# Optimization experiments

Hardware: AMD Instinct MI355X
Metric: run time of the kernel (lower is better)

The kernel has to match this reference:

```python
import jax, jax.numpy as jnp
import numpy as np

N_ATOMS = 16384
N_BLOCKS = 4096
K = 3          # top-k nearest context atoms (min(3, n_ctx) in original; n_ctx >> 3 here)
EPS_W = 1e-8   # inverse-distance weight epsilon (matches original)
EPS_D = 1e-12  # tiny epsilon inside sqrt for numerical safety of the distance


def setup_inputs() -> dict:
    key = jax.random.key(0)
    k1, k2, k3, k4, k5 = jax.random.split(key, 5)
    # coordinates spread out like real molecular coords (Angstrom-ish scale)
    X = jax.random.normal(k1, (N_ATOMS, 3), dtype=jnp.float32) * 10.0
    base_noise = jax.random.normal(k2, (N_ATOMS, 3), dtype=jnp.float32)      # randn_like(X)
    centroid_noise = jax.random.normal(k3, (N_ATOMS, 3), dtype=jnp.float32)  # per-atom randn(3)
    block_ids = jnp.sort(jax.random.randint(k4, (N_ATOMS,), 0, N_BLOCKS)).astype(jnp.int32)
    generate_mask = jax.random.randint(k5, (N_BLOCKS,), 0, 2).astype(bool)
    return {
        "X": X,
        "base_noise": base_noise,
        "centroid_noise": centroid_noise,
        "block_ids": block_ids,
        "generate_mask": generate_mask,
    }


def reference(X, base_noise, centroid_noise, block_ids, generate_mask):
    """Vectorized sample_chemical_prior: for every generated atom, find the 3
    nearest CONTEXT atoms, take an inverse-distance-weighted centroid, and add
    0.5 * gaussian noise. Non-generated atoms keep base_noise (randn_like)."""
    n = X.shape[0]
    gen_atoms = generate_mask[block_ids]           # [N] atoms being generated
    ctx = ~gen_atoms                               # [N] context atoms

    # pairwise squared distances via ||a||^2 + ||b||^2 - 2 a.b  -> [N, N]
    xn = jnp.sum(X * X, axis=-1)
    sq = xn[:, None] + xn[None, :] - 2.0 * (X @ X.T)
    d = jnp.sqrt(jnp.maximum(sq, 0.0) + EPS_D)

    # only context atoms are valid neighbor candidates; exclude self for safety
    not_self = ~jnp.eye(n, dtype=bool)
    d = jnp.where(ctx[None, :] & not_self, d, jnp.inf)

    # k nearest context atoms per row (smallest distances)
    neg_dk, idx = jax.lax.top_k(-d, K)             # [N, K]
    dk = -neg_dk

    # inverse-distance weights, normalized (matches original)
    w = 1.0 / (dk + EPS_W)
    w = w / jnp.sum(w, axis=-1, keepdims=True)

    coords = X[idx]                                # [N, K, 3] gather neighbor coords
    centroid = jnp.sum(coords * w[..., None], axis=1)  # [N, 3]

    x0 = jnp.where(gen_atoms[:, None], centroid + 0.5 * centroid_noise, base_noise)
    return x0
```

## Files before the change

kernel.cpp:

```cpp
#include <hip/hip_runtime.h>
#include <cstdint>

#define N_ATOMS 16384
#define NBLK 64
#define NTHR 256
#define G 24
#define NCELLS 13824
#define NCELLS_PAD 14336
#define CPT 14
#define BOX_LO -48.0f
#define INV_CELL 0.25f
#define SINIT 3.0e38f

#define OFF_COUNTS 0
#define OFF_ACELL 256
#define OFF_START 33280
#define OFF_GENIDX 90880
#define OFF_CTX4 156672

__device__ __forceinline__ int cell1(float x) {
    int c = (int)floorf((x - BOX_LO) * INV_CELL);
    return min(max(c, 0), G - 1);
}

__device__ __forceinline__ void ins3(float v, int vi,
                                     float& s1, float& s2, float& s3,
                                     int& i1, int& i2, int& i3)
{
    const bool b1 = v < s1, b2 = v < s2, b3 = v < s3;
    s3 = b2 ? s2 : (b3 ? v : s3);   i3 = b2 ? i2 : (b3 ? vi : i3);
    s2 = b1 ? s1 : (b2 ? v : s2);   i2 = b1 ? i1 : (b2 ? vi : i2);
    s1 = b1 ? v : s1;               i1 = b1 ? vi : i1;
}

__global__ __launch_bounds__(NTHR)
void k1_classify(const float* __restrict__ X,
                 const int* __restrict__ block_ids,
                 const unsigned int* __restrict__ mask,
                 const float* __restrict__ base_noise,
                 float* __restrict__ out,
                 unsigned short* __restrict__ acell)
{
    __shared__ int sflag;
    const int t = threadIdx.x;

    if (t == 0) sflag = 0;
    __syncthreads();
    if (mask[t] > 1u) sflag = 1;
    __syncthreads();
    const bool is_u8 = (sflag != 0);
    const unsigned char* m8 = (const unsigned char*)mask;

    const int i = blockIdx.x * NTHR + t;
    const int bid = block_ids[i];
    const bool g = is_u8 ? (m8[bid] != 0) : (mask[bid] != 0u);

    out[3 * i + 0] = base_noise[3 * i + 0];
    out[3 * i + 1] = base_noise[3 * i + 1];
    out[3 * i + 2] = base_noise[3 * i + 2];

    unsigned short c = 0xFFFFu;
    if (!g) {
        const float x = X[3 * i], y = X[3 * i + 1], z = X[3 * i + 2];
        c = (unsigned short)((cell1(z) * G + cell1(y)) * G + cell1(x));
    }
    acell[i] = c;
}

__global__ __launch_bounds__(1024)
void k2_sortscatter(const float* __restrict__ X,
                    const unsigned short* __restrict__ acell,
                    int* __restrict__ cell_start,
                    int* __restrict__ counts,
                    int* __restrict__ genidx,
                    float4* __restrict__ ctx4s)
{
    __shared__ int hist[NCELLS_PAD];
    __shared__ int wsum[16], wexc[16];
    __shared__ int gcnt;
    const int t = threadIdx.x;
    const int wave = t >> 6, lane = t & 63;

    #pragma unroll
    for (int k = 0; k < CPT; ++k) hist[t * CPT + k] = 0;
    if (t == 0) gcnt = 0;
    __syncthreads();

    #pragma unroll
    for (int it = 0; it < N_ATOMS / 1024; ++it) {
        const unsigned short c = acell[it * 1024 + t];
        if (c != 0xFFFFu) atomicAdd(&hist[c], 1);
    }
    __syncthreads();

    int loc[CPT]; int sum = 0;
    #pragma unroll
    for (int k = 0; k < CPT; ++k) {
        const int v = hist[t * CPT + k];
        loc[k] = sum; sum += v;
    }
    int v = sum;
    #pragma unroll
    for (int d = 1; d < 64; d <<= 1) { const int u = __shfl_up(v, d); if (lane >= d) v += u; }
    if (lane == 63) wsum[wave] = v;
    __syncthreads();
    if (t < 16) {
        int v2 = wsum[t];
        const int orig = v2;
        #pragma unroll
        for (int d = 1; d < 16; d <<= 1) { const int u = __shfl_up(v2, d); if (t >= d) v2 += u; }
        wexc[t] = v2 - orig;
    }
    __syncthreads();
    const int base = wexc[wave] + (v - sum);
    #pragma unroll
    for (int k = 0; k < CPT; ++k) {
        const int st = base + loc[k];
        cell_start[t * CPT + k] = st;
        hist[t * CPT + k] = st;
    }
    if (t == 1023) cell_start[NCELLS_PAD] = base + sum;
    __syncthreads();

    #pragma unroll
    for (int it = 0; it < N_ATOMS / 1024; ++it) {
        const int i = it * 1024 + t;
        const unsigned short c = acell[i];
        if (c != 0xFFFFu) {
            const int p = atomicAdd(&hist[c], 1);
            const float x = X[3 * i], y = X[3 * i + 1], z = X[3 * i + 2];
            float xn = x * x; xn += y * y; xn += z * z;
            ctx4s[p] = make_float4(x, y, z, xn);
        } else {
            genidx[atomicAdd(&gcnt, 1)] = i;
        }
    }
    __syncthreads();
    if (t == 0) { counts[1] = gcnt; counts[0] = N_ATOMS - gcnt; }
}

__global__ __launch_bounds__(NTHR)
void k4_search(const float* __restrict__ X,
               const float* __restrict__ cnoise,
               const int* __restrict__ counts,
               const int* __restrict__ cell_start,
               const float4* __restrict__ ctx4s,
               const int* __restrict__ genidx,
               float* __restrict__ out)
{
    const int n_gen = counts[1];
    const int wave = threadIdx.x >> 6, lane = threadIdx.x & 63;
    if ((int)blockIdx.x * 4 >= n_gen) return;
    const int slot = (int)blockIdx.x * 4 + wave;
    if (slot >= n_gen) return;

    const int ai = genidx[slot];
    const float qx = X[3 * ai], qy = X[3 * ai + 1], qz = X[3 * ai + 2];
    float xnq = qx * qx; xnq += qy * qy; xnq += qz * qz;
    const int cqx = cell1(qx), cqy = cell1(qy), cqz = cell1(qz);

    float s1 = SINIT, s2 = SINIT, s3 = SINIT;
    int i1 = 0, i2 = 0, i3 = 0;

    {
        int st = 0, cnt = 0;
        if (lane < 9) {
            const int dy = lane % 3 - 1, dz = lane / 3 - 1;
            const int cy = cqy + dy, cz = cqz + dz;
            if ((unsigned)cy < G && (unsigned)cz < G) {
                const int xlo = max(cqx - 1, 0), xhi = min(cqx + 1, G - 1);
                const int c0 = (cz * G + cy) * G + xlo;
                st = cell_start[c0];
                cnt = cell_start[c0 + (xhi - xlo + 1)] - st;
            }
        }
        int stv[9], base[10];
        base[0] = 0;
        #pragma unroll
        for (int k = 0; k < 9; ++k) {
            stv[k] = __builtin_amdgcn_readlane(st, k);
            base[k + 1] = base[k] + __builtin_amdgcn_readlane(cnt, k);
        }
        const int T = base[9];
        const int nro = (T + 63) >> 6;
        if (nro > 0) {
            auto calcP = [&](int j) -> int {
                const int jc = min(j, T - 1);
                int p = stv[0] + jc;
                #pragma unroll
                for (int k = 1; k < 9; ++k)
                    p = (jc >= base[k]) ? stv[k] + (jc - base[k]) : p;
                return p;
            };
            int p0 = calcP(lane);
            float4 cc0 = ctx4s[p0];
            for (int ro = 0; ro < nro; ++ro) {
                int p1 = p0; float4 cc1 = cc0;
                if (ro + 1 < nro) { p1 = calcP((ro + 1) * 64 + lane); cc1 = ctx4s[p1]; }
                if (ro * 64 + lane < T) {
                    const float dot = qx * cc0.x + qy * cc0.y + qz * cc0.z;
                    const float sq = (xnq + cc0.w) - 2.0f * dot;
                    ins3(sq, p0, s1, s2, s3, i1, i2, i3);
                }
                p0 = p1; cc0 = cc1;
            }
        }
    }

    const int cb = __popcll(__ballot(s1 + 0.01f < 16.0f))
                 + __popcll(__ballot(s2 + 0.01f < 16.0f))
                 + __popcll(__ballot(s3 + 0.01f < 16.0f));

    if (cb < 3) {
        s1 = SINIT; s2 = SINIT; s3 = SINIT;
        i1 = 0; i2 = 0; i3 = 0;
        const int n_ctx = counts[0];
        for (int base = 0; base < n_ctx; base += 512) {
            float4 cv0, cv1, cv2, cv3, cv4, cv5, cv6, cv7;
            const int pa0 = min(base + 0 * 64 + lane, n_ctx - 1);
            const int pa1 = min(base + 1 * 64 + lane, n_ctx - 1);
            const int pa2 = min(base + 2 * 64 + lane, n_ctx - 1);
            const int pa3 = min(base + 3 * 64 + lane, n_ctx - 1);
            const int pa4 = min(base + 4 * 64 + lane, n_ctx - 1);
            const int pa5 = min(base + 5 * 64 + lane, n_ctx - 1);
            const int pa6 = min(base + 6 * 64 + lane, n_ctx - 1);
            const int pa7 = min(base + 7 * 64 + lane, n_ctx - 1);
            cv0 = ctx4s[pa0]; cv1 = ctx4s[pa1]; cv2 = ctx4s[pa2]; cv3 = ctx4s[pa3];
            cv4 = ctx4s[pa4]; cv5 = ctx4s[pa5]; cv6 = ctx4s[pa6]; cv7 = ctx4s[pa7];
            #define TAIL_INS(K, CV, PA) \
                if (base + (K) * 64 + lane < n_ctx) { \
                    const float dot = qx * (CV).x + qy * (CV).y + qz * (CV).z; \
                    const float sq = (xnq + (CV).w) - 2.0f * dot; \
                    ins3(sq, (PA), s1, s2, s3, i1, i2, i3); \
                }
            TAIL_INS(0, cv0, pa0) TAIL_INS(1, cv1, pa1)
            TAIL_INS(2, cv2, pa2) TAIL_INS(3, cv3, pa3)
            TAIL_INS(4, cv4, pa4) TAIL_INS(5, cv5, pa5)
            TAIL_INS(6, cv6, pa6) TAIL_INS(7, cv7, pa7)
            #undef TAIL_INS
        }
    }

    #pragma unroll
    for (int m = 1; m < 64; m <<= 1) {
        const float a = __shfl_xor(s1, m); const int ja = __shfl_xor(i1, m);
        const float b = __shfl_xor(s2, m); const int jb = __shfl_xor(i2, m);
        const float c = __shfl_xor(s3, m); const int jc = __shfl_xor(i3, m);
        ins3(a, ja, s1, s2, s3, i1, i2, i3);
        ins3(b, jb, s1, s2, s3, i1, i2, i3);
        ins3(c, jc, s1, s2, s3, i1, i2, i3);
    }

    if (lane == 0) {
        const float d1 = sqrtf(fmaxf(s1, 0.0f) + 1e-12f);
        const float d2 = sqrtf(fmaxf(s2, 0.0f) + 1e-12f);
        const float d3 = sqrtf(fmaxf(s3, 0.0f) + 1e-12f);
        float w1 = 1.0f / (d1 + 1e-8f);
        float w2 = 1.0f / (d2 + 1e-8f);
        float w3 = 1.0f / (d3 + 1e-8f);
        float wsum = w1 + w2;
        wsum += w3;
        w1 /= wsum; w2 /= wsum; w3 /= wsum;
        const float4 c1 = ctx4s[i1];
        const float4 c2 = ctx4s[i2];
        const float4 c3 = ctx4s[i3];
        float cxo = w1 * c1.x + w2 * c2.x; cxo += w3 * c3.x;
        float cyo = w1 * c1.y + w2 * c2.y; cyo += w3 * c3.y;
        float czo = w1 * c1.z + w2 * c2.z; czo += w3 * c3.z;
        out[3 * ai + 0] = cxo + 0.5f * cnoise[3 * ai + 0];
        out[3 * ai + 1] = cyo + 0.5f * cnoise[3 * ai + 1];
        out[3 * ai + 2] = czo + 0.5f * cnoise[3 * ai + 2];
    }
}

extern "C" void kernel_launch(void* const* d_in, const int* in_sizes, int n_in,
                              void* d_out, int out_size, void* d_ws, size_t ws_size,
                              hipStream_t stream) {
    const float* X          = (const float*)d_in[0];
    const float* base_noise = (const float*)d_in[1];
    const float* cnoise     = (const float*)d_in[2];
    const int*   block_ids  = (const int*)d_in[3];
    const unsigned int* gmask = (const unsigned int*)d_in[4];
    float* out = (float*)d_out;

    char* ws = (char*)d_ws;
    int*    counts     = (int*)(ws + OFF_COUNTS);
    unsigned short* acell = (unsigned short*)(ws + OFF_ACELL);
    int*    cell_start = (int*)(ws + OFF_START);
    int*    genidx     = (int*)(ws + OFF_GENIDX);
    float4* ctx4s      = (float4*)(ws + OFF_CTX4);

    k1_classify<<<NBLK, NTHR, 0, stream>>>(X, block_ids, gmask, base_noise,
                                           out, acell);
    k2_sortscatter<<<1, 1024, 0, stream>>>(X, acell, cell_start, counts,
                                           genidx, ctx4s);
    k4_search<<<N_ATOMS / 4, NTHR, 0, stream>>>(X, cnoise, counts, cell_start,
                                                ctx4s, genidx, out);
}
```

Baseline: 54.49 us.

## Split single-block sort-scatter into rank pass plus parallel scatter kernel

```diff
diff --git a/kernel.cpp b/kernel.cpp
--- a/kernel.cpp
+++ b/kernel.cpp
@@ -13,10 +13,14 @@
 #define SINIT 3.0e38f
 
 #define OFF_COUNTS 0
-#define OFF_ACELL 256
-#define OFF_START 33280
-#define OFF_GENIDX 90880
-#define OFF_CTX4 156672
+#define OFF_BLKGEN 256
+#define OFF_BLKGOFF 512
+#define OFF_FLAGS 1024
+#define OFF_ACELL 3072
+#define OFF_POS 35840
+#define OFF_START 101376
+#define OFF_GENIDX 158976
+#define OFF_CTX4 224512
 
 __device__ __forceinline__ int cell1(float x) {
     int c = (int)floorf((x - BOX_LO) * INV_CELL);
@@ -39,10 +43,14 @@
                  const unsigned int* __restrict__ mask,
                  const float* __restrict__ base_noise,
                  float* __restrict__ out,
+                 unsigned long long* __restrict__ flags,
+                 int* __restrict__ blk_gen,
                  unsigned short* __restrict__ acell)
 {
     __shared__ int sflag;
+    __shared__ int wg[4];
     const int t = threadIdx.x;
+    const int wave = t >> 6, lane = t & 63;
 
     if (t == 0) sflag = 0;
     __syncthreads();
@@ -58,6 +66,11 @@
     out[3 * i + 0] = base_noise[3 * i + 0];
     out[3 * i + 1] = base_noise[3 * i + 1];
     out[3 * i + 2] = base_noise[3 * i + 2];
+
+    const unsigned long long mg = __ballot(g);
+    if (lane == 0) { flags[blockIdx.x * 4 + wave] = mg; wg[wave] = __popcll(mg); }
+    __syncthreads();
+    if (t == 0) blk_gen[blockIdx.x] = wg[0] + wg[1] + wg[2] + wg[3];
 
     unsigned short c = 0xFFFFu;
     if (!g) {
@@ -68,22 +81,20 @@
 }
 
 __global__ __launch_bounds__(1024)
-void k2_sortscatter(const float* __restrict__ X,
-                    const unsigned short* __restrict__ acell,
-                    int* __restrict__ cell_start,
-                    int* __restrict__ counts,
-                    int* __restrict__ genidx,
-                    float4* __restrict__ ctx4s)
+void k2_sort(const unsigned short* __restrict__ acell,
+             int* __restrict__ cell_start,
+             int* __restrict__ pos,
+             const int* __restrict__ blk_gen,
+             int* __restrict__ blk_goff,
+             int* __restrict__ counts)
 {
     __shared__ int hist[NCELLS_PAD];
     __shared__ int wsum[16], wexc[16];
-    __shared__ int gcnt;
     const int t = threadIdx.x;
     const int wave = t >> 6, lane = t & 63;
 
     #pragma unroll
     for (int k = 0; k < CPT; ++k) hist[t * CPT + k] = 0;
-    if (t == 0) gcnt = 0;
     __syncthreads();
 
     #pragma unroll
@@ -126,17 +137,46 @@
     for (int it = 0; it < N_ATOMS / 1024; ++it) {
         const int i = it * 1024 + t;
         const unsigned short c = acell[i];
-        if (c != 0xFFFFu) {
-            const int p = atomicAdd(&hist[c], 1);
-            const float x = X[3 * i], y = X[3 * i + 1], z = X[3 * i + 2];
-            float xn = x * x; xn += y * y; xn += z * z;
-            ctx4s[p] = make_float4(x, y, z, xn);
-        } else {
-            genidx[atomicAdd(&gcnt, 1)] = i;
-        }
-    }
-    __syncthreads();
-    if (t == 0) { counts[1] = gcnt; counts[0] = N_ATOMS - gcnt; }
+        if (c != 0xFFFFu) pos[i] = atomicAdd(&hist[c], 1);
+    }
+
+    if (t < 64) {
+        const int o = blk_gen[t];
+        int s = o;
+        #pragma unroll
+        for (int d = 1; d < 64; d <<= 1) { const int u = __shfl_up(s, d); if (t >= d) s += u; }
+        blk_goff[t] = s - o;
+        if (t == 63) { counts[1] = s; counts[0] = N_ATOMS - s; }
+    }
+}
+
+__global__ __launch_bounds__(NTHR)
+void k3_scatter(const float* __restrict__ X,
+                const unsigned long long* __restrict__ flags,
+                const int* __restrict__ blk_goff,
+                const int* __restrict__ pos,
+                float4* __restrict__ ctx4s,
+                int* __restrict__ genidx)
+{
+    const int t = threadIdx.x;
+    const int wave = t >> 6, lane = t & 63;
+    const int i = blockIdx.x * NTHR + t;
+    const unsigned long long fw = flags[blockIdx.x * 4 + wave];
+    const bool g = (fw >> lane) & 1ull;
+    if (g) {
+        int og = blk_goff[blockIdx.x];
+        #pragma unroll
+        for (int w = 0; w < 4; ++w) {
+            if (w < wave) og += __popcll(flags[blockIdx.x * 4 + w]);
+        }
+        const unsigned long long below = (1ull << lane) - 1ull;
+        og += __popcll(fw & below);
+        genidx[og] = i;
+    } else {
+        const float x = X[3 * i], y = X[3 * i + 1], z = X[3 * i + 2];
+        float xn = x * x; xn += y * y; xn += z * z;
+        ctx4s[pos[i]] = make_float4(x, y, z, xn);
+    }
 }
 
 __global__ __launch_bounds__(NTHR)
@@ -285,15 +325,19 @@
 
     char* ws = (char*)d_ws;
     int*    counts     = (int*)(ws + OFF_COUNTS);
+    int*    blk_gen    = (int*)(ws + OFF_BLKGEN);
+    int*    blk_goff   = (int*)(ws + OFF_BLKGOFF);
+    unsigned long long* flags = (unsigned long long*)(ws + OFF_FLAGS);
     unsigned short* acell = (unsigned short*)(ws + OFF_ACELL);
+    int*    pos        = (int*)(ws + OFF_POS);
     int*    cell_start = (int*)(ws + OFF_START);
     int*    genidx     = (int*)(ws + OFF_GENIDX);
     float4* ctx4s      = (float4*)(ws + OFF_CTX4);
 
     k1_classify<<<NBLK, NTHR, 0, stream>>>(X, block_ids, gmask, base_noise,
-                                           out, acell);
-    k2_sortscatter<<<1, 1024, 0, stream>>>(X, acell, cell_start, counts,
-                                           genidx, ctx4s);
+                                           out, flags, blk_gen, acell);
+    k2_sort<<<1, 1024, 0, stream>>>(acell, cell_start, pos, blk_gen, blk_goff, counts);
+    k3_scatter<<<NBLK, NTHR, 0, stream>>>(X, flags, blk_goff, pos, ctx4s, genidx);
     k4_search<<<N_ATOMS / 4, NTHR, 0, stream>>>(X, cnoise, counts, cell_start,
                                                 ctx4s, genidx, out);
 }
```

Result: faster. 50.53 us (-7.3%).
